# Kernel tuning notes

Hardware: AMD Instinct MI355X
Metric: run time of the kernel (lower is better)

## Reference

```python
import jax, jax.numpy as jnp
import numpy as np

DIM = 256
NUM_HEADS = 8
WH, WW = 7, 7
N = WH * WW
HEAD_DIM = DIM // NUM_HEADS
SCALE = HEAD_DIM ** -0.5
B_ = 4096
NW = 64  # windows per image


def _relative_position_index():
    # Swin relative position index: (N, N) int32 in [0, (2Wh-1)*(2Ww-1))
    coords = np.stack(np.meshgrid(np.arange(WH), np.arange(WW), indexing='ij'))  # (2, Wh, Ww)
    cf = coords.reshape(2, -1)  # (2, N)
    rel = cf[:, :, None] - cf[:, None, :]  # (2, N, N)
    rel = rel.transpose(1, 2, 0).copy()
    rel[:, :, 0] += WH - 1
    rel[:, :, 1] += WW - 1
    rel[:, :, 0] *= 2 * WW - 1
    return jnp.asarray(rel.sum(-1), dtype=jnp.int32)  # (N, N)


def setup_inputs() -> dict:
    key = jax.random.key(0)
    ks = jax.random.split(key, 7)
    x = jax.random.normal(ks[0], (B_, N, DIM), dtype=jnp.float32)
    mask = jax.random.normal(ks[1], (NW, N, N), dtype=jnp.float32)
    qkv_w = jax.random.normal(ks[2], (3 * DIM, DIM), dtype=jnp.float32) * 0.02
    qkv_b = jnp.zeros((3 * DIM,), dtype=jnp.float32)
    proj_w = jax.random.normal(ks[3], (DIM, DIM), dtype=jnp.float32) * 0.02
    proj_b = jnp.zeros((DIM,), dtype=jnp.float32)
    bias_table = jax.random.normal(ks[4], ((2 * WH - 1) * (2 * WW - 1), NUM_HEADS), dtype=jnp.float32) * 0.02
    rel_index = _relative_position_index()
    return {"x": x, "mask": mask, "qkv_w": qkv_w, "qkv_b": qkv_b,
            "proj_w": proj_w, "proj_b": proj_b, "bias_table": bias_table,
            "rel_index": rel_index}


def reference(x, mask, qkv_w, qkv_b, proj_w, proj_b, bias_table, rel_index):
    Bw, n, c = x.shape
    # qkv projection: (B_, N, 3C) -> (3, B_, nH, N, hd)
    qkv = (x @ qkv_w.T + qkv_b).reshape(Bw, n, 3, NUM_HEADS, HEAD_DIM)
    qkv = qkv.transpose(2, 0, 3, 1, 4)
    q, k, v = qkv[0], qkv[1], qkv[2]
    attn = jnp.einsum('bhqd,bhkd->bhqk', q * SCALE, k)  # (B_, nH, N, N)
    # gathered relative position bias: (nH, N, N)
    rpb = bias_table[rel_index.reshape(-1)].reshape(n, n, NUM_HEADS).transpose(2, 0, 1)
    attn = attn + rpb[None]
    # window mask: reshape batch into (B, nW) and broadcast mask per-window
    nW = mask.shape[0]
    attn = attn.reshape(Bw // nW, nW, NUM_HEADS, n, n) + mask[None, :, None]
    attn = attn.reshape(Bw, NUM_HEADS, n, n)
    attn = jax.nn.softmax(attn, axis=-1)
    out = jnp.einsum('bhqk,bhkd->bhqd', attn, v)  # (B_, nH, N, hd)
    out = out.transpose(0, 2, 1, 3).reshape(Bw, n, c)
    return out @ proj_w.T + proj_b
```

## Files before the change

### kernel.cpp

```cpp
#include <hip/hip_runtime.h>
#include <hip/hip_bf16.h>

typedef __bf16 bf16;
typedef __bf16 bf16x8 __attribute__((ext_vector_type(8)));
typedef float  f32x4  __attribute__((ext_vector_type(4)));
typedef float  f32x8  __attribute__((ext_vector_type(8)));

#define MFMA16(A,B,C) __builtin_amdgcn_mfma_f32_16x16x32_bf16((A),(B),(C),0,0,0)

constexpr int   N_TOK = 49;
constexpr int   DIM_C = 256;
constexpr float SCALE = 0.17677669529663687f;

constexpr int QK_STRIDE  = 512;
constexpr int P_BASE     = 49 * 512;
constexpr int P_WSTRIDE  = 49 * 64;
constexpr int XB_BASE    = P_BASE;
constexpr int VT_BASE    = P_BASE + 8 * P_WSTRIDE;
constexpr int SMEM_ELEMS = VT_BASE + 256 * 64;

constexpr size_t CB_BYTES   = 64ull * 8 * 64 * 64 * 4;
constexpr int    QKVW_ELEMS = 768 * 256;
constexpr int    PROJW_ELEMS= 256 * 256;

__global__ __launch_bounds__(256) void build_cb_kernel(
    const float* __restrict__ bias_table, const float* __restrict__ mask,
    const int* __restrict__ rel_index, float* __restrict__ cb) {
  int idx = blockIdx.x * 256 + threadIdx.x;
  int j = idx & 63, m = (idx >> 6) & 63, h = (idx >> 12) & 7, w = idx >> 15;
  float v = 0.f;
  if (j < N_TOK && m < N_TOK)
    v = bias_table[rel_index[m * 49 + j] * 8 + h] + mask[(w * 49 + m) * 49 + j];
  cb[idx] = v;
}

__global__ __launch_bounds__(256) void cvt_w_kernel(
    const float* __restrict__ qkv_w, const float* __restrict__ proj_w,
    bf16* __restrict__ qkv_wb, bf16* __restrict__ proj_wb) {
  int i = blockIdx.x * 256 + threadIdx.x;
  if (i < QKVW_ELEMS) qkv_wb[i] = (bf16)qkv_w[i];
  else                proj_wb[i - QKVW_ELEMS] = (bf16)proj_w[i - QKVW_ELEMS];
}

__global__ __launch_bounds__(512) void win_attn_kernel(
    const float* __restrict__ x, const bf16* __restrict__ qkv_wb,
    const float* __restrict__ qkv_b, const bf16* __restrict__ proj_wb,
    const float* __restrict__ proj_b, const float* __restrict__ cb,
    float* __restrict__ out) {
  __shared__ bf16 smem[SMEM_ELEMS];

  const int beta  = blockIdx.x;
  const int w_idx = beta >> 6;
  const int img   = beta & 63;
  const int b     = img * 64 + w_idx;
  const int tid   = threadIdx.x;
  const int wv    = tid >> 6;
  const int l     = tid & 63;
  const int l15   = l & 15, lgp = l >> 4;

  const f32x4 fzero = {0.f, 0.f, 0.f, 0.f};
  const bf16x8 bzero = {(bf16)0.f,(bf16)0.f,(bf16)0.f,(bf16)0.f,
                        (bf16)0.f,(bf16)0.f,(bf16)0.f,(bf16)0.f};

  for (int i = tid; i < 256 * 15; i += 512) {
    int d = i / 15, j = 49 + i % 15;
    smem[VT_BASE + d * 64 + (j ^ ((d & 7) << 3))] = (bf16)0.f;
  }

  const float* xg = x + (size_t)b * (N_TOK * DIM_C);
  for (int c = tid; c < (N_TOK * DIM_C / 8); c += 512) {
    int m = c >> 5, k0 = (c & 31) * 8;
    f32x8 f = *reinterpret_cast<const f32x8*>(xg + m * 256 + k0);
    bf16x8 v;
#pragma unroll
    for (int e = 0; e < 8; ++e) v[e] = (bf16)f[e];
    *reinterpret_cast<bf16x8*>(&smem[XB_BASE + m * 256 + (k0 ^ ((m & 7) << 3))]) = v;
  }
  __syncthreads();

  for (int ntg = 0; ntg < 2; ++ntg) {
    f32x4 acc[3][4];
    for (int t = 0; t < 3; ++t)
      for (int mt = 0; mt < 4; ++mt) acc[t][mt] = fzero;
    for (int k0 = 0; k0 < 8; ++k0) {
      const int kk = k0 * 32 + lgp * 8;
      bf16x8 A[4];
#pragma unroll
      for (int mt = 0; mt < 4; ++mt) {
        int m = mt * 16 + l15;
        A[mt] = (m < N_TOK)
            ? *reinterpret_cast<const bf16x8*>(
                  &smem[XB_BASE + m * 256 + (kk ^ ((m & 7) << 3))])
            : bzero;
      }
#pragma unroll
      for (int t = 0; t < 3; ++t) {
        int n = (wv * 6 + ntg * 3 + t) * 16 + l15;
        bf16x8 B = *reinterpret_cast<const bf16x8*>(qkv_wb + n * DIM_C + kk);
#pragma unroll
        for (int mt = 0; mt < 4; ++mt) acc[t][mt] = MFMA16(A[mt], B, acc[t][mt]);
      }
    }
#pragma unroll
    for (int t = 0; t < 3; ++t) {
      int c = (wv * 6 + ntg * 3 + t) * 16 + l15;
      float qb = qkv_b[c];
#pragma unroll
      for (int mt = 0; mt < 4; ++mt) {
#pragma unroll
        for (int r = 0; r < 4; ++r) {
          int m = mt * 16 + lgp * 4 + r;
          if (m < N_TOK) {
            float v = acc[t][mt][r] + qb;
            if (c < 512) {
              float vs = (c < 256) ? v * SCALE : v;
              smem[m * QK_STRIDE + (c ^ ((m & 7) << 3))] = (bf16)vs;
            } else {
              int d = c - 512;
              smem[VT_BASE + d * 64 + (m ^ ((d & 7) << 3))] = (bf16)v;
            }
          }
        }
      }
    }
  }
  __syncthreads();

  const int h = wv;
  bf16* pbuf = smem + P_BASE + wv * P_WSTRIDE;

  f32x4 s[4][4];
  {
    bf16x8 A[4], B[4];
#pragma unroll
    for (int mt = 0; mt < 4; ++mt) {
      int m = mt * 16 + l15;
      A[mt] = *reinterpret_cast<const bf16x8*>(
          &smem[m * QK_STRIDE + ((h * 32 + lgp * 8) ^ ((m & 7) << 3))]);
    }
#pragma unroll
    for (int jt = 0; jt < 4; ++jt) {
      int n = jt * 16 + l15;
      B[jt] = *reinterpret_cast<const bf16x8*>(
          &smem[n * QK_STRIDE + ((256 + h * 32 + lgp * 8) ^ ((n & 7) << 3))]);
    }
#pragma unroll
    for (int mt = 0; mt < 4; ++mt)
#pragma unroll
      for (int jt = 0; jt < 4; ++jt) s[mt][jt] = MFMA16(A[mt], B[jt], fzero);
  }

  const float* cbp = cb + ((size_t)(w_idx * 8 + h)) * 64 * 64;
  float rinv[4][4];
#pragma unroll
  for (int mt = 0; mt < 4; ++mt) {
    float lgt[4][4];
#pragma unroll
    for (int jt = 0; jt < 4; ++jt) {
      int jc = jt * 16 + l15;
#pragma unroll
      for (int r = 0; r < 4; ++r) {
        int m = mt * 16 + lgp * 4 + r;
        float v = s[mt][jt][r] + cbp[m * 64 + jc];
        if (jc >= N_TOK) v = -3.0e38f;
        lgt[jt][r] = v;
      }
    }
#pragma unroll
    for (int r = 0; r < 4; ++r) {
      float mx = fmaxf(fmaxf(lgt[0][r], lgt[1][r]), fmaxf(lgt[2][r], lgt[3][r]));
      mx = fmaxf(mx, __shfl_xor(mx, 1));
      mx = fmaxf(mx, __shfl_xor(mx, 2));
      mx = fmaxf(mx, __shfl_xor(mx, 4));
      mx = fmaxf(mx, __shfl_xor(mx, 8));
      float sum = 0.f;
#pragma unroll
      for (int jt = 0; jt < 4; ++jt) {
        float e = __expf(lgt[jt][r] - mx);
        lgt[jt][r] = e;
        sum += e;
      }
      sum += __shfl_xor(sum, 1);
      sum += __shfl_xor(sum, 2);
      sum += __shfl_xor(sum, 4);
      sum += __shfl_xor(sum, 8);
      rinv[mt][r] = 1.0f / sum;
      int m = mt * 16 + lgp * 4 + r;
      if (m < N_TOK) {
#pragma unroll
        for (int jt = 0; jt < 4; ++jt) {
          int j = jt * 16 + l15;
          pbuf[m * 64 + (j ^ ((m & 7) << 3))] = (bf16)lgt[jt][r];
        }
      }
    }
  }

#pragma unroll
  for (int mt = 0; mt < 4; ++mt) {
#pragma unroll
    for (int dt = 0; dt < 2; ++dt) {
      f32x4 acc = fzero;
#pragma unroll
      for (int ks = 0; ks < 2; ++ks) {
        int m = mt * 16 + l15;
        bf16x8 A = *reinterpret_cast<const bf16x8*>(
            &pbuf[m * 64 + ((ks * 32 + lgp * 8) ^ ((m & 7) << 3))]);
        int d = h * 32 + dt * 16 + l15;
        bf16x8 B = *reinterpret_cast<const bf16x8*>(
            &smem[VT_BASE + d * 64 + ((ks * 32 + lgp * 8) ^ ((d & 7) << 3))]);
        acc = MFMA16(A, B, acc);
      }
#pragma unroll
      for (int r = 0; r < 4; ++r) {
        int m = mt * 16 + lgp * 4 + r;
        if (m < N_TOK) {
          int c = h * 32 + dt * 16 + l15;
          smem[m * QK_STRIDE + (c ^ ((m & 7) << 3))] = (bf16)(acc[r] * rinv[mt][r]);
        }
      }
    }
  }
  __syncthreads();

  f32x4 acc2[2][4];
  for (int ci = 0; ci < 2; ++ci)
    for (int mt = 0; mt < 4; ++mt) acc2[ci][mt] = fzero;
  for (int k0 = 0; k0 < 8; ++k0) {
    int kk = k0 * 32 + lgp * 8;
    bf16x8 A[4];
#pragma unroll
    for (int mt = 0; mt < 4; ++mt) {
      int m = mt * 16 + l15;
      A[mt] = *reinterpret_cast<const bf16x8*>(
          &smem[m * QK_STRIDE + (kk ^ ((m & 7) << 3))]);
    }
#pragma unroll
    for (int ci = 0; ci < 2; ++ci) {
      int n = (wv * 2 + ci) * 16 + l15;
      bf16x8 B = *reinterpret_cast<const bf16x8*>(proj_wb + n * DIM_C + kk);
#pragma unroll
      for (int mt = 0; mt < 4; ++mt) acc2[ci][mt] = MFMA16(A[mt], B, acc2[ci][mt]);
    }
  }
  float* ob = out + (size_t)b * (N_TOK * DIM_C);
#pragma unroll
  for (int ci = 0; ci < 2; ++ci) {
    int c = (wv * 2 + ci) * 16 + l15;
    float pb = proj_b[c];
#pragma unroll
    for (int mt = 0; mt < 4; ++mt) {
#pragma unroll
      for (int r = 0; r < 4; ++r) {
        int m = mt * 16 + lgp * 4 + r;
        if (m < N_TOK) ob[m * DIM_C + c] = acc2[ci][mt][r] + pb;
      }
    }
  }
}

extern "C" void kernel_launch(void* const* d_in, const int* in_sizes, int n_in,
                              void* d_out, int out_size, void* d_ws, size_t ws_size,
                              hipStream_t stream) {
  const float* x          = (const float*)d_in[0];
  const float* mask       = (const float*)d_in[1];
  const float* qkv_w      = (const float*)d_in[2];
  const float* qkv_b      = (const float*)d_in[3];
  const float* proj_w     = (const float*)d_in[4];
  const float* proj_b     = (const float*)d_in[5];
  const float* bias_table = (const float*)d_in[6];
  const int*   rel_index  = (const int*)d_in[7];

  float* cb      = (float*)d_ws;
  bf16*  qkv_wb  = (bf16*)((char*)d_ws + CB_BYTES);
  bf16*  proj_wb = (bf16*)((char*)d_ws + CB_BYTES + QKVW_ELEMS*2);

  hipLaunchKernelGGL(build_cb_kernel, dim3(8192), dim3(256), 0, stream,
                     bias_table, mask, rel_index, cb);
  hipLaunchKernelGGL(cvt_w_kernel, dim3(1024), dim3(256), 0, stream,
                     qkv_w, proj_w, qkv_wb, proj_wb);
  hipLaunchKernelGGL(win_attn_kernel, dim3(4096), dim3(512), 0, stream,
                     x, qkv_wb, qkv_b, proj_wb, proj_b, cb, (float*)d_out);
}
```

Baseline: 463.4 us.

## Compact shared-memory layout and split QKV GEMM to raise occupancy

Shrinks the LDS footprint of the window-attention kernel. The x tile, the V transpose and the attention output now alias one region, and the softmax probabilities are stored in the dead Q/K columns instead of a separate per-head buffer. The QKV GEMM is split into a Q/K pass and a V pass so the V results can overwrite the x tile after a barrier. QK^T is computed per row tile to cut live registers, and launch bounds request 4 blocks per CU. The aim is higher occupancy, at the cost of an extra barrier and unaligned 4-wide LDS reads in the projection.

After: 463.6 us. No clear change (+0.0%).

```diff
diff --git a/kernel.cpp b/kernel.cpp
--- a/kernel.cpp
+++ b/kernel.cpp
@@ -2,6 +2,7 @@
 #include <hip/hip_bf16.h>
 
 typedef __bf16 bf16;
+typedef __bf16 bf16x4 __attribute__((ext_vector_type(4)));
 typedef __bf16 bf16x8 __attribute__((ext_vector_type(8)));
 typedef float  f32x4  __attribute__((ext_vector_type(4)));
 typedef float  f32x8  __attribute__((ext_vector_type(8)));
@@ -12,16 +13,13 @@
 constexpr int   DIM_C = 256;
 constexpr float SCALE = 0.17677669529663687f;
 
-constexpr int QK_STRIDE  = 512;
-constexpr int P_BASE     = 49 * 512;
-constexpr int P_WSTRIDE  = 49 * 64;
-constexpr int XB_BASE    = P_BASE;
-constexpr int VT_BASE    = P_BASE + 8 * P_WSTRIDE;
-constexpr int SMEM_ELEMS = VT_BASE + 256 * 64;
-
-constexpr size_t CB_BYTES   = 64ull * 8 * 64 * 64 * 4;
-constexpr int    QKVW_ELEMS = 768 * 256;
-constexpr int    PROJW_ELEMS= 256 * 256;
+constexpr int VT         = 25088;
+constexpr int PAD_BASE   = VT + 256 * 56;
+constexpr int SMEM_ELEMS = PAD_BASE + 512;
+
+constexpr size_t CB_BYTES    = 64ull * 8 * 64 * 64 * 4;
+constexpr int    QKVW_ELEMS  = 768 * 256;
+constexpr int    PROJW_ELEMS = 256 * 256;
 
 __global__ __launch_bounds__(256) void build_cb_kernel(
     const float* __restrict__ bias_table, const float* __restrict__ mask,
@@ -42,7 +40,7 @@
   else                proj_wb[i - QKVW_ELEMS] = (bf16)proj_w[i - QKVW_ELEMS];
 }
 
-__global__ __launch_bounds__(512) void win_attn_kernel(
+__global__ __launch_bounds__(512, 4) void win_attn_kernel(
     const float* __restrict__ x, const bf16* __restrict__ qkv_wb,
     const float* __restrict__ qkv_b, const bf16* __restrict__ proj_wb,
     const float* __restrict__ proj_b, const float* __restrict__ cb,
@@ -62,9 +60,10 @@
   const bf16x8 bzero = {(bf16)0.f,(bf16)0.f,(bf16)0.f,(bf16)0.f,
                         (bf16)0.f,(bf16)0.f,(bf16)0.f,(bf16)0.f};
 
-  for (int i = tid; i < 256 * 15; i += 512) {
-    int d = i / 15, j = 49 + i % 15;
-    smem[VT_BASE + d * 64 + (j ^ ((d & 7) << 3))] = (bf16)0.f;
+  if (tid < 512) smem[PAD_BASE + tid] = (bf16)0.f;
+  if (tid < 224) {
+    int d = 224 + tid / 7, j = 49 + tid % 7;
+    smem[VT + d * 56 + j] = (bf16)0.f;
   }
 
   const float* xg = x + (size_t)b * (N_TOK * DIM_C);
@@ -74,14 +73,15 @@
     bf16x8 v;
 #pragma unroll
     for (int e = 0; e < 8; ++e) v[e] = (bf16)f[e];
-    *reinterpret_cast<bf16x8*>(&smem[XB_BASE + m * 256 + (k0 ^ ((m & 7) << 3))]) = v;
+    *reinterpret_cast<bf16x8*>(&smem[VT + m * 256 + (k0 ^ ((m & 7) << 3))]) = v;
   }
   __syncthreads();
 
-  for (int ntg = 0; ntg < 2; ++ntg) {
-    f32x4 acc[3][4];
-    for (int t = 0; t < 3; ++t)
-      for (int mt = 0; mt < 4; ++mt) acc[t][mt] = fzero;
+  {
+    f32x4 acc[4][4];
+#pragma unroll
+    for (int i = 0; i < 4; ++i)
+      for (int mt = 0; mt < 4; ++mt) acc[i][mt] = fzero;
     for (int k0 = 0; k0 < 8; ++k0) {
       const int kk = k0 * 32 + lgp * 8;
       bf16x8 A[4];
@@ -90,35 +90,169 @@
         int m = mt * 16 + l15;
         A[mt] = (m < N_TOK)
             ? *reinterpret_cast<const bf16x8*>(
-                  &smem[XB_BASE + m * 256 + (kk ^ ((m & 7) << 3))])
+                  &smem[VT + m * 256 + (kk ^ ((m & 7) << 3))])
             : bzero;
       }
 #pragma unroll
-      for (int t = 0; t < 3; ++t) {
-        int n = (wv * 6 + ntg * 3 + t) * 16 + l15;
-        bf16x8 B = *reinterpret_cast<const bf16x8*>(qkv_wb + n * DIM_C + kk);
-#pragma unroll
-        for (int mt = 0; mt < 4; ++mt) acc[t][mt] = MFMA16(A[mt], B, acc[t][mt]);
-      }
-    }
-#pragma unroll
-    for (int t = 0; t < 3; ++t) {
-      int c = (wv * 6 + ntg * 3 + t) * 16 + l15;
+      for (int i = 0; i < 4; ++i) {
+        int c = (4 * wv + i) * 16 + l15;
+        bf16x8 B = *reinterpret_cast<const bf16x8*>(qkv_wb + c * DIM_C + kk);
+#pragma unroll
+        for (int mt = 0; mt < 4; ++mt) acc[i][mt] = MFMA16(A[mt], B, acc[i][mt]);
+      }
+    }
+#pragma unroll
+    for (int i = 0; i < 4; ++i) {
+      int c = (4 * wv + i) * 16 + l15;
       float qb = qkv_b[c];
+      float sc = (c < 256) ? SCALE : 1.0f;
 #pragma unroll
       for (int mt = 0; mt < 4; ++mt) {
+#pragma unroll
+        for (int r = 0; r < 4; ++r) {
+          int m = mt * 16 + lgp * 4 + r;
+          if (m < N_TOK)
+            smem[m * 512 + (c ^ ((m & 7) << 3))] = (bf16)((acc[i][mt][r] + qb) * sc);
+        }
+      }
+    }
+  }
+
+  {
+    f32x4 accv[2][4];
+#pragma unroll
+    for (int i = 0; i < 2; ++i)
+      for (int mt = 0; mt < 4; ++mt) accv[i][mt] = fzero;
+    for (int k0 = 0; k0 < 8; ++k0) {
+      const int kk = k0 * 32 + lgp * 8;
+      bf16x8 A[4];
+#pragma unroll
+      for (int mt = 0; mt < 4; ++mt) {
+        int m = mt * 16 + l15;
+        A[mt] = (m < N_TOK)
+            ? *reinterpret_cast<const bf16x8*>(
+                  &smem[VT + m * 256 + (kk ^ ((m & 7) << 3))])
+            : bzero;
+      }
+#pragma unroll
+      for (int i = 0; i < 2; ++i) {
+        int c = (32 + 2 * wv + i) * 16 + l15;
+        bf16x8 B = *reinterpret_cast<const bf16x8*>(qkv_wb + c * DIM_C + kk);
+#pragma unroll
+        for (int mt = 0; mt < 4; ++mt) accv[i][mt] = MFMA16(A[mt], B, accv[i][mt]);
+      }
+    }
+    __syncthreads();
+#pragma unroll
+    for (int i = 0; i < 2; ++i) {
+      int c = (32 + 2 * wv + i) * 16 + l15;
+      int d = c - 512;
+      float qb = qkv_b[c];
+#pragma unroll
+      for (int mt = 0; mt < 4; ++mt) {
+#pragma unroll
+        for (int r = 0; r < 4; ++r) {
+          int m = mt * 16 + lgp * 4 + r;
+          if (m < N_TOK) smem[VT + d * 56 + m] = (bf16)(accv[i][mt][r] + qb);
+        }
+      }
+    }
+  }
+  __syncthreads();
+
+  const int h = wv;
+  float rinv[4][4];
+  {
+    bf16x8 Bk[4];
+#pragma unroll
+    for (int jt = 0; jt < 4; ++jt) {
+      int n = jt * 16 + l15;
+      Bk[jt] = *reinterpret_cast<const bf16x8*>(
+          &smem[n * 512 + ((256 + h * 32 + lgp * 8) ^ ((n & 7) << 3))]);
+    }
+    const float* cbp = cb + ((size_t)(w_idx * 8 + h)) * 64 * 64;
+#pragma unroll
+    for (int mt = 0; mt < 4; ++mt) {
+      int m_a = mt * 16 + l15;
+      bf16x8 Aq = *reinterpret_cast<const bf16x8*>(
+          &smem[m_a * 512 + ((h * 32 + lgp * 8) ^ ((m_a & 7) << 3))]);
+      f32x4 s4[4];
+#pragma unroll
+      for (int jt = 0; jt < 4; ++jt) s4[jt] = MFMA16(Aq, Bk[jt], fzero);
+      float lgt[4][4];
+#pragma unroll
+      for (int jt = 0; jt < 4; ++jt) {
+        int jc = jt * 16 + l15;
+#pragma unroll
+        for (int r = 0; r < 4; ++r) {
+          int m = mt * 16 + lgp * 4 + r;
+          float v = s4[jt][r] + cbp[m * 64 + jc];
+          if (jc >= N_TOK) v = -3.0e38f;
+          lgt[jt][r] = v;
+        }
+      }
+#pragma unroll
+      for (int r = 0; r < 4; ++r) {
+        float mx = fmaxf(fmaxf(lgt[0][r], lgt[1][r]), fmaxf(lgt[2][r], lgt[3][r]));
+        mx = fmaxf(mx, __shfl_xor(mx, 1));
+        mx = fmaxf(mx, __shfl_xor(mx, 2));
+        mx = fmaxf(mx, __shfl_xor(mx, 4));
+        mx = fmaxf(mx, __shfl_xor(mx, 8));
+        float sum = 0.f;
+#pragma unroll
+        for (int jt = 0; jt < 4; ++jt) {
+          float e = __expf(lgt[jt][r] - mx);
+          lgt[jt][r] = e;
+          sum += e;
+        }
+        sum += __shfl_xor(sum, 1);
+        sum += __shfl_xor(sum, 2);
+        sum += __shfl_xor(sum, 4);
+        sum += __shfl_xor(sum, 8);
+        rinv[mt][r] = 1.0f / sum;
+        int m = mt * 16 + lgp * 4 + r;
+        if (m < N_TOK) {
+#pragma unroll
+          for (int jt = 0; jt < 4; ++jt) {
+            int j = jt * 16 + l15;
+            int c = (j < 32) ? (h * 32 + j) : (224 + h * 32 + j);
+            smem[m * 512 + (c ^ ((m & 7) << 3))] = (bf16)lgt[jt][r];
+          }
+        }
+      }
+    }
+  }
+
+  {
+    bf16x8 Vf[2][2];
+#pragma unroll
+    for (int dt = 0; dt < 2; ++dt)
+#pragma unroll
+      for (int ks = 0; ks < 2; ++ks) {
+        int d = h * 32 + dt * 16 + l15;
+        Vf[dt][ks] = *reinterpret_cast<const bf16x8*>(
+            &smem[VT + d * 56 + ks * 32 + lgp * 8]);
+      }
+#pragma unroll
+    for (int mt = 0; mt < 4; ++mt) {
+      int m_a = mt * 16 + l15;
+      bf16x8 Ap[2];
+#pragma unroll
+      for (int ks = 0; ks < 2; ++ks) {
+        int c0 = (ks == 0) ? (h * 32 + lgp * 8) : (256 + h * 32 + lgp * 8);
+        Ap[ks] = *reinterpret_cast<const bf16x8*>(
+            &smem[m_a * 512 + (c0 ^ ((m_a & 7) << 3))]);
+      }
+#pragma unroll
+      for (int dt = 0; dt < 2; ++dt) {
+        f32x4 acc = MFMA16(Ap[0], Vf[dt][0], fzero);
+        acc = MFMA16(Ap[1], Vf[dt][1], acc);
 #pragma unroll
         for (int r = 0; r < 4; ++r) {
           int m = mt * 16 + lgp * 4 + r;
           if (m < N_TOK) {
-            float v = acc[t][mt][r] + qb;
-            if (c < 512) {
-              float vs = (c < 256) ? v * SCALE : v;
-              smem[m * QK_STRIDE + (c ^ ((m & 7) << 3))] = (bf16)vs;
-            } else {
-              int d = c - 512;
-              smem[VT_BASE + d * 64 + (m ^ ((d & 7) << 3))] = (bf16)v;
-            }
+            int dd = dt * 16 + l15;
+            smem[VT + h * 1792 + m * 36 + dd] = (bf16)(acc[r] * rinv[mt][r]);
           }
         }
       }
@@ -126,119 +260,25 @@
   }
   __syncthreads();
 
-  const int h = wv;
-  bf16* pbuf = smem + P_BASE + wv * P_WSTRIDE;
-
-  f32x4 s[4][4];
-  {
-    bf16x8 A[4], B[4];
-#pragma unroll
-    for (int mt = 0; mt < 4; ++mt) {
-      int m = mt * 16 + l15;
-      A[mt] = *reinterpret_cast<const bf16x8*>(
-          &smem[m * QK_STRIDE + ((h * 32 + lgp * 8) ^ ((m & 7) << 3))]);
-    }
-#pragma unroll
-    for (int jt = 0; jt < 4; ++jt) {
-      int n = jt * 16 + l15;
-      B[jt] = *reinterpret_cast<const bf16x8*>(
-          &smem[n * QK_STRIDE + ((256 + h * 32 + lgp * 8) ^ ((n & 7) << 3))]);
-    }
-#pragma unroll
-    for (int mt = 0; mt < 4; ++mt)
-#pragma unroll
-      for (int jt = 0; jt < 4; ++jt) s[mt][jt] = MFMA16(A[mt], B[jt], fzero);
-  }
-
-  const float* cbp = cb + ((size_t)(w_idx * 8 + h)) * 64 * 64;
-  float rinv[4][4];
-#pragma unroll
-  for (int mt = 0; mt < 4; ++mt) {
-    float lgt[4][4];
-#pragma unroll
-    for (int jt = 0; jt < 4; ++jt) {
-      int jc = jt * 16 + l15;
-#pragma unroll
-      for (int r = 0; r < 4; ++r) {
-        int m = mt * 16 + lgp * 4 + r;
-        float v = s[mt][jt][r] + cbp[m * 64 + jc];
-        if (jc >= N_TOK) v = -3.0e38f;
-        lgt[jt][r] = v;
-      }
-    }
-#pragma unroll
-    for (int r = 0; r < 4; ++r) {
-      float mx = fmaxf(fmaxf(lgt[0][r], lgt[1][r]), fmaxf(lgt[2][r], lgt[3][r]));
-      mx = fmaxf(mx, __shfl_xor(mx, 1));
-      mx = fmaxf(mx, __shfl_xor(mx, 2));
-      mx = fmaxf(mx, __shfl_xor(mx, 4));
-      mx = fmaxf(mx, __shfl_xor(mx, 8));
-      float sum = 0.f;
-#pragma unroll
-      for (int jt = 0; jt < 4; ++jt) {
-        float e = __expf(lgt[jt][r] - mx);
-        lgt[jt][r] = e;
-        sum += e;
-      }
-      sum += __shfl_xor(sum, 1);
-      sum += __shfl_xor(sum, 2);
-      sum += __shfl_xor(sum, 4);
-      sum += __shfl_xor(sum, 8);
-      rinv[mt][r] = 1.0f / sum;
-      int m = mt * 16 + lgp * 4 + r;
-      if (m < N_TOK) {
-#pragma unroll
-        for (int jt = 0; jt < 4; ++jt) {
-          int j = jt * 16 + l15;
-          pbuf[m * 64 + (j ^ ((m & 7) << 3))] = (bf16)lgt[jt][r];
-        }
-      }
-    }
-  }
-
-#pragma unroll
-  for (int mt = 0; mt < 4; ++mt) {
-#pragma unroll
-    for (int dt = 0; dt < 2; ++dt) {
-      f32x4 acc = fzero;
-#pragma unroll
-      for (int ks = 0; ks < 2; ++ks) {
-        int m = mt * 16 + l15;
-        bf16x8 A = *reinterpret_cast<const bf16x8*>(
-            &pbuf[m * 64 + ((ks * 32 + lgp * 8) ^ ((m & 7) << 3))]);
-        int d = h * 32 + dt * 16 + l15;
-        bf16x8 B = *reinterpret_cast<const bf16x8*>(
-            &smem[VT_BASE + d * 64 + ((ks * 32 + lgp * 8) ^ ((d & 7) << 3))]);
-        acc = MFMA16(A, B, acc);
-      }
-#pragma unroll
-      for (int r = 0; r < 4; ++r) {
-        int m = mt * 16 + lgp * 4 + r;
-        if (m < N_TOK) {
-          int c = h * 32 + dt * 16 + l15;
-          smem[m * QK_STRIDE + (c ^ ((m & 7) << 3))] = (bf16)(acc[r] * rinv[mt][r]);
-        }
-      }
-    }
-  }
-  __syncthreads();
-
   f32x4 acc2[2][4];
+#pragma unroll
   for (int ci = 0; ci < 2; ++ci)
     for (int mt = 0; mt < 4; ++mt) acc2[ci][mt] = fzero;
   for (int k0 = 0; k0 < 8; ++k0) {
-    int kk = k0 * 32 + lgp * 8;
     bf16x8 A[4];
 #pragma unroll
     for (int mt = 0; mt < 4; ++mt) {
       int m = mt * 16 + l15;
-      A[mt] = *reinterpret_cast<const bf16x8*>(
-          &smem[m * QK_STRIDE + (kk ^ ((m & 7) << 3))]);
+      int base = VT + k0 * 1792 + m * 36 + lgp * 8;
+      bf16x4 lo = *reinterpret_cast<const bf16x4*>(&smem[base]);
+      bf16x4 hi = *reinterpret_cast<const bf16x4*>(&smem[base + 4]);
+      A[mt] = __builtin_shufflevector(lo, hi, 0, 1, 2, 3, 4, 5, 6, 7);
     }
 #pragma unroll
     for (int ci = 0; ci < 2; ++ci) {
       int n = (wv * 2 + ci) * 16 + l15;
-      bf16x8 B = *reinterpret_cast<const bf16x8*>(proj_wb + n * DIM_C + kk);
+      bf16x8 B = *reinterpret_cast<const bf16x8*>(
+          proj_wb + n * DIM_C + k0 * 32 + lgp * 8);
 #pragma unroll
       for (int mt = 0; mt < 4; ++mt) acc2[ci][mt] = MFMA16(A[mt], B, acc2[ci][mt]);
     }
@@ -273,7 +313,7 @@
 
   float* cb      = (float*)d_ws;
   bf16*  qkv_wb  = (bf16*)((char*)d_ws + CB_BYTES);
-  bf16*  proj_wb = (bf16*)((char*)d_ws + CB_BYTES + QKVW_ELEMS*2);
+  bf16*  proj_wb = (bf16*)((char*)d_ws + CB_BYTES + QKVW_ELEMS * 2);
 
   hipLaunchKernelGGL(build_cb_kernel, dim3(8192), dim3(256), 0, stream,
                      bias_table, mask, rel_index, cb);
```
